# Performance work log

Measured on AMD Instinct MI355X. Metric: run time of the kernel, lower is better.

## Reference

```python
import jax, jax.numpy as jnp
import numpy as np

N_QUBITS = 10
EMBED_DIM = 512
FFN_DIM = 2048
DIM = 2 ** N_QUBITS


def _apply_rx(state, theta, wire):
    # state: (N, 2^n) complex64; theta: scalar or (N,)
    N = state.shape[0]
    hi = 2 ** wire                      # dims before the wire axis (wire 0 = MSB)
    lo = 2 ** (N_QUBITS - 1 - wire)
    s = state.reshape(N, hi, 2, lo)
    th = jnp.asarray(theta, jnp.float32).reshape(-1, 1, 1)  # (N,1,1) or (1,1,1)
    c = jnp.cos(th / 2).astype(jnp.complex64)
    ms = (-1j * jnp.sin(th / 2)).astype(jnp.complex64)
    s0, s1 = s[:, :, 0, :], s[:, :, 1, :]
    out = jnp.stack([c * s0 + ms * s1, ms * s0 + c * s1], axis=2)
    return out.reshape(N, DIM)


def _apply_cnot(state, ctrl, tgt):
    N = state.shape[0]
    s = state.reshape((N,) + (2,) * N_QUBITS)
    s0 = jax.lax.index_in_dim(s, 0, axis=ctrl + 1, keepdims=True)
    s1 = jax.lax.index_in_dim(s, 1, axis=ctrl + 1, keepdims=True)
    s1 = jnp.flip(s1, axis=tgt + 1)  # X on target where control == 1
    return jnp.concatenate([s0, s1], axis=ctrl + 1).reshape(N, DIM)


def _pauliz_signs():
    idx = np.arange(DIM)
    bits = (idx[:, None] >> (N_QUBITS - 1 - np.arange(N_QUBITS))[None, :]) & 1
    return jnp.asarray(1.0 - 2.0 * bits, jnp.float32)  # (2^n, n)


def _quantum_layer(tokens, rx_params):
    # tokens: (N, embed_dim); uses first n_qubits features as encoder angles
    N = tokens.shape[0]
    state = jnp.zeros((N, DIM), jnp.complex64).at[:, 0].set(1.0)
    for w in range(N_QUBITS):                    # encoder: RX(x_w) on wire w
        state = _apply_rx(state, tokens[:, w], w)
    for w in range(N_QUBITS):                    # trainable RX per wire
        state = _apply_rx(state, rx_params[w], w)
    for w in range(N_QUBITS - 1):                # CNOT chain
        state = _apply_cnot(state, w, w + 1)
    state = _apply_cnot(state, N_QUBITS - 1, 0)  # wrap-around CNOT
    probs = state.real ** 2 + state.imag ** 2    # (N, 2^n)
    return probs @ _pauliz_signs()               # (N, n_qubits) <Z_w>


def setup_inputs() -> dict:
    key = jax.random.key(0)
    ks = jax.random.split(key, 6)
    x = jax.random.normal(ks[0], (16, 1024, EMBED_DIM), jnp.float32)
    rx_params = jax.random.normal(ks[1], (N_QUBITS,), jnp.float32)
    lim1 = 1.0 / np.sqrt(N_QUBITS)
    w1 = jax.random.uniform(ks[2], (FFN_DIM, N_QUBITS), jnp.float32, -lim1, lim1)
    b1 = jax.random.uniform(ks[3], (FFN_DIM,), jnp.float32, -lim1, lim1)
    lim2 = 1.0 / np.sqrt(FFN_DIM)
    w2 = jax.random.uniform(ks[4], (EMBED_DIM, FFN_DIM), jnp.float32, -lim2, lim2)
    b2 = jax.random.uniform(ks[5], (EMBED_DIM,), jnp.float32, -lim2, lim2)
    return {"x": x, "rx_params": rx_params, "w1": w1, "b1": b1, "w2": w2, "b2": b2}


def reference(x, rx_params, w1, b1, w2, b2):
    B, S, _ = x.shape
    q_out = _quantum_layer(x.reshape(B * S, EMBED_DIM), rx_params)
    q_out = q_out.reshape(B, S, N_QUBITS)
    h = jax.nn.relu(q_out @ w1.T + b1)           # dropout is identity in eval
    return h @ w2.T + b2
```

## Files before the change

kernel.cpp:

```cpp
#include <hip/hip_runtime.h>
#include <hip/hip_bf16.h>
#include <math.h>


typedef __attribute__((ext_vector_type(8))) short short8;
typedef __attribute__((ext_vector_type(8))) unsigned short ushort8;
typedef __attribute__((ext_vector_type(4))) float fx4;

constexpr int EDIM = 512;
constexpr int FDIM = 2048;
constexpr int NQ   = 10;
constexpr int BK   = 64;
constexpr int BM   = 128;
constexpr int BN   = 128;
constexpr int CSTR = 8192;
constexpr int NGSTR = 262144;
constexpr int W2P_UNITS = EDIM * FDIM / 8;

__device__ __forceinline__ ushort f2bf(float f) {
    union { float f; unsigned u; } v; v.f = f;
    unsigned u = v.u + 0x7FFFu + ((v.u >> 16) & 1u);
    return (ushort)(u >> 16);
}
__device__ __forceinline__ float bf2f(ushort u) {
    union { unsigned u; float f; } v; v.u = (unsigned)u << 16; return v.f;
}
__device__ __forceinline__ unsigned cvtpk(float lo, float hi) {
    unsigned r;
    asm("v_cvt_pk_bf16_f32 %0, %1, %2" : "=v"(r) : "v"(lo), "v"(hi));
    return r;
}

__global__ void prep(const float* __restrict__ w2, const float* __restrict__ w1,
                     const float* __restrict__ b1,
                     ushort* __restrict__ w2p, ushort* __restrict__ w1t) {
    int gid = blockIdx.x * blockDim.x + threadIdx.x;
    int np  = gridDim.x * blockDim.x;
    for (int u = gid; u < W2P_UNITS; u += np) {
        int l16 = u & 15, quad = (u >> 4) & 3, hf = (u >> 6) & 1;
        int nt = (u >> 7) & 3, wn = (u >> 9) & 1, c = (u >> 10) & 31, ng = u >> 15;
        int row = ng * 128 + wn * 64 + nt * 16 + l16;
        int col = c * 64 + (hf * 4 + quad) * 8;
        const float* src = w2 + (size_t)row * FDIM + col;
        float4 a = *(const float4*)src;
        float4 b = *(const float4*)(src + 4);
        ushort8 o;
        o[0] = f2bf(a.x); o[1] = f2bf(a.y); o[2] = f2bf(a.z); o[3] = f2bf(a.w);
        o[4] = f2bf(b.x); o[5] = f2bf(b.y); o[6] = f2bf(b.z); o[7] = f2bf(b.w);
        *(ushort8*)&w2p[(size_t)u * 8] = o;
    }
    for (int f = gid; f < FDIM; f += np) {
        ushort zr[32];
        #pragma unroll
        for (int w = 0; w < NQ; ++w) {
            float v  = w1[f * NQ + w];
            ushort hb = f2bf(v);
            ushort lb = f2bf(v - bf2f(hb));
            zr[w] = hb; zr[10 + w] = hb; zr[20 + w] = lb;
        }
        float bv  = b1[f];
        ushort bh = f2bf(bv);
        zr[30] = bh; zr[31] = f2bf(bv - bf2f(bh));
        #pragma unroll
        for (int u = 0; u < 4; ++u)
            *(ushort8*)&w1t[f * 32 + u * 8] = *(ushort8*)&zr[u * 8];
    }
}

__global__ __launch_bounds__(256, 2) void fused(
    const float* __restrict__ x, const float* __restrict__ rx,
    const ushort* __restrict__ w1t,
    const ushort* __restrict__ w2p,
    const float* __restrict__ b2,
    float* __restrict__ out)
{
    __shared__ __align__(16) ushort Zs[BM * 32];
    __shared__ __align__(16) ushort As[2][BM * BK];

    const int tid = threadIdx.x;
    const int m0  = blockIdx.x * BM;
    const int n0  = blockIdx.y * BN;

    if (tid < BM) {
        const float* xr = x + (size_t)(m0 + tid) * EDIM;
        float4 xa = *(const float4*)xr;
        float4 xb = *(const float4*)(xr + 4);
        float2 xc = *(const float2*)(xr + 8);
        float xv[NQ] = {xa.x, xa.y, xa.z, xa.w, xb.x, xb.y, xb.z, xb.w, xc.x, xc.y};
        float c[NQ], q[NQ];
        #pragma unroll
        for (int w = 0; w < NQ; ++w) c[w] = cosf(xv[w] + rx[w]);
        float p0 = c[1];
        #pragma unroll
        for (int w = 2; w < NQ; ++w) p0 *= c[w];
        q[0] = p0;
        float p = c[0];
        #pragma unroll
        for (int w = 1; w < NQ; ++w) { p *= c[w]; q[w] = p; }
        ushort zr[32];
        #pragma unroll
        for (int w = 0; w < NQ; ++w) {
            ushort hb = f2bf(q[w]);
            ushort lb = f2bf(q[w] - bf2f(hb));
            zr[w] = hb; zr[10 + w] = lb; zr[20 + w] = hb;
        }
        zr[30] = 0x3F80u; zr[31] = 0x3F80u;
        #pragma unroll
        for (int u = 0; u < 4; ++u)
            *(ushort8*)&Zs[tid * 32 + u * 8] = *(ushort8*)&zr[u * 8];
    }
    __syncthreads();

    const int wave = tid >> 6, lane = tid & 63;
    const int quad = lane >> 4, l16 = lane & 15;
    const int wm   = wave >> 1, wn = wave & 1;
    const int swz  = l16 & 7;

    const int hm0 = (wave & 1) * 64;
    const int hf0 = (wave >> 1) * 32;
    short8 zf[4];
    #pragma unroll
    for (int mi = 0; mi < 4; ++mi)
        zf[mi] = *(const short8*)&Zs[(hm0 + mi * 16 + l16) * 32 + quad * 8];

    const ushort* gB = w2p + (size_t)blockIdx.y * NGSTR + wn * 4096 + lane * 8;

    int aro[4];
    #pragma unroll
    for (int t = 0; t < 4; ++t)
        aro[t] = (wm * 64 + t * 16 + l16) * BK;

    fx4 acc[4][4];
    #pragma unroll
    for (int a = 0; a < 4; ++a)
        #pragma unroll
        for (int b = 0; b < 4; ++b) acc[a][b] = fx4{0.f, 0.f, 0.f, 0.f};

    const fx4 zacc = fx4{0.f, 0.f, 0.f, 0.f};

    short8 wfE[2], wfO[2];
    uint2  pE[4][2], pO[4][2];
    short8 bfE[4][2], bfO[4][2];

#define WLOAD(WF, CH) do { _Pragma("unroll") \
    for (int fi = 0; fi < 2; ++fi) \
        WF[fi] = *(const short8*)(w1t + ((CH) * 64 + hf0 + fi * 16 + l16) * 32 + quad * 8); \
} while (0)

#define BLOAD(BFR) do { _Pragma("unroll") \
    for (int nt = 0; nt < 4; ++nt) { \
        BFR[nt][0] = *(const short8*)(gB + nt * 1024); \
        BFR[nt][1] = *(const short8*)(gB + nt * 1024 + 512); \
    } \
    gB += CSTR; \
} while (0)

#define HCALC(P, WF) do { _Pragma("unroll") \
    for (int mi = 0; mi < 4; ++mi) \
        _Pragma("unroll") \
        for (int fi = 0; fi < 2; ++fi) { \
            fx4 hv = __builtin_amdgcn_mfma_f32_16x16x32_bf16( \
                WF[fi], zf[mi], zacc, 0, 0, 0); \
            unsigned ua = cvtpk(fmaxf(hv[0], 0.f), fmaxf(hv[1], 0.f)); \
            unsigned ub = cvtpk(fmaxf(hv[2], 0.f), fmaxf(hv[3], 0.f)); \
            P[mi][fi] = make_uint2(ua, ub); \
        } \
} while (0)

#define HWRITE(BUF, P) do { _Pragma("unroll") \
    for (int mi = 0; mi < 4; ++mi) { \
        const int hrow = hm0 + mi * 16 + l16; \
        ushort* arow = &As[BUF][hrow * BK]; \
        _Pragma("unroll") \
        for (int fi = 0; fi < 2; ++fi) { \
            const int blk = (hf0 >> 3) + fi * 2 + (quad >> 1); \
            *(uint2*)&arow[((blk ^ swz) << 3) + ((quad & 1) << 2)] = P[mi][fi]; \
        } \
    } \
} while (0)

#define COMPUTE(BUF, BFR) do { \
    short8 af[4][2]; \
    _Pragma("unroll") \
    for (int t = 0; t < 4; ++t) \
        _Pragma("unroll") \
        for (int hf = 0; hf < 2; ++hf) \
            af[t][hf] = *(const short8*)&As[BUF][aro[t] + (((hf * 4 + quad) ^ swz) << 3)]; \
    __builtin_amdgcn_s_setprio(1); \
    _Pragma("unroll") \
    for (int hf = 0; hf < 2; ++hf) \
        _Pragma("unroll") \
        for (int mt = 0; mt < 4; ++mt) \
            _Pragma("unroll") \
            for (int nt = 0; nt < 4; ++nt) \
                acc[mt][nt] = __builtin_amdgcn_mfma_f32_16x16x32_bf16( \
                    af[mt][hf], BFR[nt][hf], acc[mt][nt], 0, 0, 0); \
    __builtin_amdgcn_s_setprio(0); \
} while (0)

    WLOAD(wfE, 0); WLOAD(wfO, 1);
    BLOAD(bfE);
    HCALC(pE, wfE); HWRITE(0, pE);
    HCALC(pO, wfO);
    WLOAD(wfE, 2); WLOAD(wfO, 3);
    __syncthreads();

    for (int p = 0; p < 14; ++p) {
        BLOAD(bfO);
        HWRITE(1, pO); HCALC(pE, wfE); WLOAD(wfE, 2 * p + 4);
        COMPUTE(0, bfE);
        __syncthreads();
        BLOAD(bfE);
        HWRITE(0, pE); HCALC(pO, wfO); WLOAD(wfO, 2 * p + 5);
        COMPUTE(1, bfO);
        __syncthreads();
    }
    BLOAD(bfO);
    HWRITE(1, pO); HCALC(pE, wfE);
    COMPUTE(0, bfE); __syncthreads();
    BLOAD(bfE);
    HWRITE(0, pE); HCALC(pO, wfO);
    COMPUTE(1, bfO); __syncthreads();
    BLOAD(bfO);
    HWRITE(1, pO);
    COMPUTE(0, bfE); __syncthreads();
    COMPUTE(1, bfO);

#undef COMPUTE
#undef HWRITE
#undef HCALC
#undef BLOAD
#undef WLOAD

    float bb[4];
    #pragma unroll
    for (int nt = 0; nt < 4; ++nt) bb[nt] = b2[n0 + wn * 64 + nt * 16 + l16];
    #pragma unroll
    for (int mt = 0; mt < 4; ++mt) {
        const int mbase = m0 + wm * 64 + mt * 16 + quad * 4;
        #pragma unroll
        for (int nt = 0; nt < 4; ++nt) {
            const int n = n0 + wn * 64 + nt * 16 + l16;
            #pragma unroll
            for (int r = 0; r < 4; ++r)
                out[(size_t)(mbase + r) * EDIM + n] = acc[mt][nt][r] + bb[nt];
        }
    }
}

extern "C" void kernel_launch(void* const* d_in, const int* in_sizes, int n_in,
                              void* d_out, int out_size, void* d_ws, size_t ws_size,
                              hipStream_t stream) {
    const float* x  = (const float*)d_in[0];
    const float* rx = (const float*)d_in[1];
    const float* w1 = (const float*)d_in[2];
    const float* b1 = (const float*)d_in[3];
    const float* w2 = (const float*)d_in[4];
    const float* b2 = (const float*)d_in[5];
    float* out = (float*)d_out;

    const int M = in_sizes[0] / EDIM;

    ushort* w2p = (ushort*)d_ws;
    ushort* w1t = (ushort*)((char*)d_ws + (size_t)EDIM * FDIM * 2);
    (void)ws_size; (void)n_in; (void)out_size;

    hipLaunchKernelGGL(prep, dim3(256), dim3(256), 0, stream, w2, w1, b1, w2p, w1t);
    hipLaunchKernelGGL(fused, dim3(M / BM, EDIM / BN), dim3(256), 0, stream,
                       x, rx, w1t, w2p, b2, out);
}
```

Baseline: 129.3 us.

## Give each wave a private hidden-activation LDS buffer, removing block barriers

Each wave now computes the full 64-wide hidden chunk for its own 64 rows into a private LDS slice, so the second GEMM reads only data that wave wrote. This removes all __syncthreads from the main loop. The cost is that waves sharing the same rows compute the same hidden activations twice, doubling first-layer MFMA work, and LDS use grows from 32KB to 64KB per block. The larger LDS footprint may reduce occupancy under launch_bounds(256,2).

```diff
diff --git a/kernel.cpp b/kernel.cpp
--- a/kernel.cpp
+++ b/kernel.cpp
@@ -75,7 +75,7 @@
     float* __restrict__ out)
 {
     __shared__ __align__(16) ushort Zs[BM * 32];
-    __shared__ __align__(16) ushort As[2][BM * BK];
+    __shared__ __align__(16) ushort As[2 * 4 * 4096];
 
     const int tid = threadIdx.x;
     const int m0  = blockIdx.x * BM;
@@ -116,19 +116,20 @@
     const int wm   = wave >> 1, wn = wave & 1;
     const int swz  = l16 & 7;
 
-    const int hm0 = (wave & 1) * 64;
-    const int hf0 = (wave >> 1) * 32;
     short8 zf[4];
     #pragma unroll
     for (int mi = 0; mi < 4; ++mi)
-        zf[mi] = *(const short8*)&Zs[(hm0 + mi * 16 + l16) * 32 + quad * 8];
+        zf[mi] = *(const short8*)&Zs[(wm * 64 + mi * 16 + l16) * 32 + quad * 8];
 
     const ushort* gB = w2p + (size_t)blockIdx.y * NGSTR + wn * 4096 + lane * 8;
+    const ushort* gW = w1t + l16 * 32 + quad * 8;
 
     int aro[4];
     #pragma unroll
     for (int t = 0; t < 4; ++t)
-        aro[t] = (wm * 64 + t * 16 + l16) * BK;
+        aro[t] = (t * 16 + l16) * BK;
+    ushort* wavebuf0 = &As[(0 * 4 + wave) * 4096];
+    ushort* wavebuf1 = &As[(1 * 4 + wave) * 4096];
 
     fx4 acc[4][4];
     #pragma unroll
@@ -138,13 +139,12 @@
 
     const fx4 zacc = fx4{0.f, 0.f, 0.f, 0.f};
 
-    short8 wfE[2], wfO[2];
-    uint2  pE[4][2], pO[4][2];
+    short8 wfE[4], wfO[4];
     short8 bfE[4][2], bfO[4][2];
 
-#define WLOAD(WF, CH) do { _Pragma("unroll") \
-    for (int fi = 0; fi < 2; ++fi) \
-        WF[fi] = *(const short8*)(w1t + ((CH) * 64 + hf0 + fi * 16 + l16) * 32 + quad * 8); \
+#define WLOAD(WF) do { _Pragma("unroll") \
+    for (int fi = 0; fi < 4; ++fi) WF[fi] = *(const short8*)(gW + fi * 512); \
+    gW += 2048; \
 } while (0)
 
 #define BLOAD(BFR) do { _Pragma("unroll") \
@@ -155,37 +155,31 @@
     gB += CSTR; \
 } while (0)
 
-#define HCALC(P, WF) do { _Pragma("unroll") \
-    for (int mi = 0; mi < 4; ++mi) \
-        _Pragma("unroll") \
-        for (int fi = 0; fi < 2; ++fi) { \
-            fx4 hv = __builtin_amdgcn_mfma_f32_16x16x32_bf16( \
+#define HPROD(WB, WF) do { _Pragma("unroll") \
+    for (int fi = 0; fi < 4; ++fi) { \
+        fx4 hv[4]; \
+        _Pragma("unroll") \
+        for (int mi = 0; mi < 4; ++mi) \
+            hv[mi] = __builtin_amdgcn_mfma_f32_16x16x32_bf16( \
                 WF[fi], zf[mi], zacc, 0, 0, 0); \
-            unsigned ua = cvtpk(fmaxf(hv[0], 0.f), fmaxf(hv[1], 0.f)); \
-            unsigned ub = cvtpk(fmaxf(hv[2], 0.f), fmaxf(hv[3], 0.f)); \
-            P[mi][fi] = make_uint2(ua, ub); \
-        } \
-} while (0)
-
-#define HWRITE(BUF, P) do { _Pragma("unroll") \
-    for (int mi = 0; mi < 4; ++mi) { \
-        const int hrow = hm0 + mi * 16 + l16; \
-        ushort* arow = &As[BUF][hrow * BK]; \
-        _Pragma("unroll") \
-        for (int fi = 0; fi < 2; ++fi) { \
-            const int blk = (hf0 >> 3) + fi * 2 + (quad >> 1); \
-            *(uint2*)&arow[((blk ^ swz) << 3) + ((quad & 1) << 2)] = P[mi][fi]; \
+        _Pragma("unroll") \
+        for (int mi = 0; mi < 4; ++mi) { \
+            unsigned ua = cvtpk(fmaxf(hv[mi][0], 0.f), fmaxf(hv[mi][1], 0.f)); \
+            unsigned ub = cvtpk(fmaxf(hv[mi][2], 0.f), fmaxf(hv[mi][3], 0.f)); \
+            const int blk = fi * 2 + (quad >> 1); \
+            *(uint2*)&(WB)[(mi * 16 + l16) * BK + ((blk ^ swz) << 3) + ((quad & 1) << 2)] \
+                = make_uint2(ua, ub); \
         } \
     } \
 } while (0)
 
-#define COMPUTE(BUF, BFR) do { \
+#define COMPUTE(RB, BFR) do { \
     short8 af[4][2]; \
     _Pragma("unroll") \
     for (int t = 0; t < 4; ++t) \
         _Pragma("unroll") \
         for (int hf = 0; hf < 2; ++hf) \
-            af[t][hf] = *(const short8*)&As[BUF][aro[t] + (((hf * 4 + quad) ^ swz) << 3)]; \
+            af[t][hf] = *(const short8*)&(RB)[aro[t] + (((hf * 4 + quad) ^ swz) << 3)]; \
     __builtin_amdgcn_s_setprio(1); \
     _Pragma("unroll") \
     for (int hf = 0; hf < 2; ++hf) \
@@ -198,37 +192,26 @@
     __builtin_amdgcn_s_setprio(0); \
 } while (0)
 
-    WLOAD(wfE, 0); WLOAD(wfO, 1);
-    BLOAD(bfE);
-    HCALC(pE, wfE); HWRITE(0, pE);
-    HCALC(pO, wfO);
-    WLOAD(wfE, 2); WLOAD(wfO, 3);
-    __syncthreads();
-
-    for (int p = 0; p < 14; ++p) {
+    WLOAD(wfE); BLOAD(bfE);
+    HPROD(wavebuf0, wfE);
+    WLOAD(wfO); BLOAD(bfO);
+    HPROD(wavebuf1, wfO);
+
+    for (int p = 0; p < 15; ++p) {
+        WLOAD(wfE);
+        COMPUTE(wavebuf0, bfE);
+        BLOAD(bfE);
+        HPROD(wavebuf0, wfE);
+        WLOAD(wfO);
+        COMPUTE(wavebuf1, bfO);
         BLOAD(bfO);
-        HWRITE(1, pO); HCALC(pE, wfE); WLOAD(wfE, 2 * p + 4);
-        COMPUTE(0, bfE);
-        __syncthreads();
-        BLOAD(bfE);
-        HWRITE(0, pE); HCALC(pO, wfO); WLOAD(wfO, 2 * p + 5);
-        COMPUTE(1, bfO);
-        __syncthreads();
-    }
-    BLOAD(bfO);
-    HWRITE(1, pO); HCALC(pE, wfE);
-    COMPUTE(0, bfE); __syncthreads();
-    BLOAD(bfE);
-    HWRITE(0, pE); HCALC(pO, wfO);
-    COMPUTE(1, bfO); __syncthreads();
-    BLOAD(bfO);
-    HWRITE(1, pO);
-    COMPUTE(0, bfE); __syncthreads();
-    COMPUTE(1, bfO);
+        HPROD(wavebuf1, wfO);
+    }
+    COMPUTE(wavebuf0, bfE);
+    COMPUTE(wavebuf1, bfO);
 
 #undef COMPUTE
-#undef HWRITE
-#undef HCALC
+#undef HPROD
 #undef BLOAD
 #undef WLOAD
 
```

Result: slower. 136.8 us (+5.8%).
